# Kernel optimization log

Measured on AMD Instinct MI355X. Metric: run time of the kernel, lower is better.

## Reference

```python
import jax, jax.numpy as jnp
import numpy as np

L, B, H = 4096, 32, 512


def setup_inputs() -> dict:
    key = jax.random.key(0)
    k1, k2, k3, k4 = jax.random.split(key, 4)
    query = jax.random.normal(k1, (B, H), dtype=jnp.float32)
    key_val = jax.random.normal(k2, (L, B, H), dtype=jnp.float32)
    # torch Linear(2H, H, bias=False): weight is (H, 2H); we store transposed (2H, H)
    W = jax.random.normal(k3, (2 * H, H), dtype=jnp.float32) * (1.0 / np.sqrt(2 * H))
    v = jax.random.normal(k4, (H,), dtype=jnp.float32)
    return {"query": query, "key_val": key_val, "W": W, "v": v}


def reference(query, key_val, W, v):
    # concat([expand(query), key], -1) @ W == query @ W_q + key @ W_k
    Wq, Wk = W[:H], W[H:]                       # each (H, H)
    q_proj = query @ Wq                          # (B, H)
    k_proj = jnp.einsum('lbi,ih->lbh', key_val, Wk)  # (L, B, H)
    energy = jnp.tanh(q_proj[None, :, :] + k_proj)   # (L, B, H)
    scores = jnp.einsum('h,lbh->bl', v, energy)      # (B, L)
    return jax.nn.softmax(scores, axis=1)[:, None, :]  # (B, 1, L)
```

## Files before the change

### kernel.cpp

```cpp
#include <hip/hip_runtime.h>
#include <hip/hip_bf16.h>
#include <stdint.h>

#define L_DIM 4096
#define B_DIM 32
#define H_DIM 512
#define M_DIM (L_DIM * B_DIM)
#define K_DIM H_DIM

typedef _Float16 half8 __attribute__((ext_vector_type(8)));
typedef __fp16 fp16x2 __attribute__((ext_vector_type(2)));
typedef float floatx4 __attribute__((ext_vector_type(4)));

__device__ __forceinline__ float tanh_fast(float x) {
  float e = __builtin_amdgcn_exp2f(x * 2.88539008177793f);
  return 1.0f - 2.0f * __builtin_amdgcn_rcpf(e + 1.0f);
}

__device__ __forceinline__ void async_copy16(const _Float16* g, _Float16* l) {
  __builtin_amdgcn_global_load_lds(
      (__attribute__((address_space(1))) unsigned int*)(const_cast<_Float16*>(g)),
      (__attribute__((address_space(3))) unsigned int*)(l),
      16, 0, 0);
}

__global__ __launch_bounds__(128) void qproj_kernel(const float* __restrict__ query,
                                                    const float* __restrict__ W,
                                                    float* __restrict__ qp) {
  const int b = blockIdx.x;
  const int h = threadIdx.x * 4;
  const float* qrow = query + b * H_DIM;
  float4 acc = make_float4(0.f, 0.f, 0.f, 0.f);
#pragma unroll 8
  for (int i = 0; i < K_DIM; ++i) {
    const float qv = qrow[i];
    const float4 w4 = *(const float4*)(W + (size_t)i * H_DIM + h);
    acc.x += qv * w4.x; acc.y += qv * w4.y;
    acc.z += qv * w4.z; acc.w += qv * w4.w;
  }
  *(float4*)(qp + (size_t)b * H_DIM + h) = acc;
}

__global__ __launch_bounds__(256) void wconv_kernel(const float* __restrict__ W,
                                                    _Float16* __restrict__ W2) {
  const int t = blockIdx.x * 256 + threadIdx.x;
  const int s = t & 3;
  const int n = (t >> 2) & 511;
  const int kt = t >> 11;
  const int kseg = s ^ ((n >> 1) & 3);
  const int kbase = H_DIM + kt * 32 + kseg * 8;
  half8 h;
#pragma unroll
  for (int j = 0; j < 8; ++j)
    h[j] = (_Float16)W[(size_t)(kbase + j) * H_DIM + n];
  *(half8*)(W2 + (size_t)t * 8) = h;
}

__global__ __launch_bounds__(256, 2) void fused_gemm_kernel(
    const float* __restrict__ key, const _Float16* __restrict__ W2,
    const float* __restrict__ qp, const float* __restrict__ v,
    float* __restrict__ scores) {
  __shared__ __align__(16) _Float16 As[64 * 40];
  __shared__ __align__(16) _Float16 Bs[512 * 32];
  __shared__ float swave[256];

  const int tid = threadIdx.x;
  const int lane = tid & 63;
  const int w = tid >> 6;
  const int l15 = lane & 15;
  const int quad = lane >> 4;
  const int m0 = blockIdx.x * 64;

  const int am = tid >> 2;
  const int aks = (tid & 3) * 8;
  const float* ag = key + (size_t)(m0 + am) * K_DIM + aks;
  _Float16* asdst = As + am * 40 + aks;

  const _Float16* bg = W2 + (size_t)(w * 64 + lane) * 8;
  _Float16* bdst0 = Bs + (size_t)(w * 64) * 8;

  int aoff[4];
#pragma unroll
  for (int fm = 0; fm < 4; ++fm) aoff[fm] = (fm * 16 + l15) * 40 + quad * 8;
  int boff[8];
#pragma unroll
  for (int fn = 0; fn < 8; ++fn) {
    const int n = w * 128 + fn * 16 + l15;
    boff[fn] = n * 32 + (quad ^ ((n >> 1) & 3)) * 8;
  }

  floatx4 acc[4][8];
#pragma unroll
  for (int fm = 0; fm < 4; ++fm)
#pragma unroll
    for (int fn = 0; fn < 8; ++fn) acc[fm][fn] = (floatx4)0.0f;

  for (int kt = 0; kt < 16; ++kt) {
    const float4 f0 = *(const float4*)(ag + kt * 32);
    const float4 f1 = *(const float4*)(ag + kt * 32 + 4);
    __syncthreads();
    const fp16x2 p0 = __builtin_amdgcn_cvt_pkrtz(f0.x, f0.y);
    const fp16x2 p1 = __builtin_amdgcn_cvt_pkrtz(f0.z, f0.w);
    const fp16x2 p2 = __builtin_amdgcn_cvt_pkrtz(f1.x, f1.y);
    const fp16x2 p3 = __builtin_amdgcn_cvt_pkrtz(f1.z, f1.w);
    uint4 u;
    u.x = __builtin_bit_cast(unsigned, p0);
    u.y = __builtin_bit_cast(unsigned, p1);
    u.z = __builtin_bit_cast(unsigned, p2);
    u.w = __builtin_bit_cast(unsigned, p3);
    *(uint4*)asdst = u;
    const _Float16* bsrc = bg + (size_t)kt * 16384;
#pragma unroll
    for (int c = 0; c < 8; ++c) async_copy16(bsrc + c * 2048, bdst0 + c * 2048);
    __syncthreads();

    half8 av[4];
#pragma unroll
    for (int fm = 0; fm < 4; ++fm) av[fm] = *(const half8*)(As + aoff[fm]);
    half8 bv[8];
#pragma unroll
    for (int fn = 0; fn < 8; ++fn) bv[fn] = *(const half8*)(Bs + boff[fn]);
#pragma unroll
    for (int fm = 0; fm < 4; ++fm)
#pragma unroll
      for (int fn = 0; fn < 8; ++fn)
        acc[fm][fn] = __builtin_amdgcn_mfma_f32_16x16x32_f16(av[fm], bv[fn],
                                                             acc[fm][fn], 0, 0, 0);
  }

  float vv[8];
#pragma unroll
  for (int fn = 0; fn < 8; ++fn) vv[fn] = v[w * 128 + fn * 16 + l15];

#pragma unroll
  for (int fm = 0; fm < 4; ++fm) {
#pragma unroll
    for (int r = 0; r < 4; ++r) {
      const int mrow = fm * 16 + quad * 4 + r;
      const float* qrow = qp + (size_t)(mrow & 31) * H_DIM;
      float rs = 0.f;
#pragma unroll
      for (int fn = 0; fn < 8; ++fn) {
        const int n = w * 128 + fn * 16 + l15;
        const float x = qrow[n] + acc[fm][fn][r];
        rs += vv[fn] * tanh_fast(x);
      }
      rs += __shfl_xor(rs, 1);
      rs += __shfl_xor(rs, 2);
      rs += __shfl_xor(rs, 4);
      rs += __shfl_xor(rs, 8);
      if (l15 == 0) swave[w * 64 + mrow] = rs;
    }
  }
  __syncthreads();
  if (tid < 64) {
    const float s = swave[tid] + swave[64 + tid] + swave[128 + tid] + swave[192 + tid];
    scores[(size_t)m0 + tid] = s;
  }
}

__global__ __launch_bounds__(256) void softmax_kernel(const float* __restrict__ scores,
                                                      float* __restrict__ out) {
  const int b = blockIdx.x;
  const int t = threadIdx.x;
  __shared__ float red[256];
  float s[16];
#pragma unroll
  for (int i = 0; i < 16; ++i) s[i] = scores[(size_t)(t + i * 256) * B_DIM + b];
  float mx = s[0];
#pragma unroll
  for (int i = 1; i < 16; ++i) mx = fmaxf(mx, s[i]);
  red[t] = mx;
  __syncthreads();
  for (int off = 128; off > 0; off >>= 1) {
    if (t < off) red[t] = fmaxf(red[t], red[t + off]);
    __syncthreads();
  }
  mx = red[0];
  __syncthreads();
  float sum = 0.f;
#pragma unroll
  for (int i = 0; i < 16; ++i) {
    s[i] = __builtin_amdgcn_exp2f((s[i] - mx) * 1.44269504f);
    sum += s[i];
  }
  red[t] = sum;
  __syncthreads();
  for (int off = 128; off > 0; off >>= 1) {
    if (t < off) red[t] += red[t + off];
    __syncthreads();
  }
  const float inv = 1.0f / red[0];
#pragma unroll
  for (int i = 0; i < 16; ++i) out[(size_t)b * L_DIM + t + i * 256] = s[i] * inv;
}

extern "C" void kernel_launch(void* const* d_in, const int* in_sizes, int n_in,
                              void* d_out, int out_size, void* d_ws, size_t ws_size,
                              hipStream_t stream) {
  const float* query = (const float*)d_in[0];
  const float* key   = (const float*)d_in[1];
  const float* W     = (const float*)d_in[2];
  const float* v     = (const float*)d_in[3];
  float* out = (float*)d_out;

  char* ws = (char*)d_ws;
  float* qp       = (float*)ws;
  float* scores   = (float*)(ws + 65536);
  _Float16* W2    = (_Float16*)(ws + 65536 + 524288);

  qproj_kernel<<<32, 128, 0, stream>>>(query, W, qp);
  wconv_kernel<<<128, 256, 0, stream>>>(W, W2);
  fused_gemm_kernel<<<M_DIM / 64, 256, 0, stream>>>(key, W2, qp, v, scores);
  softmax_kernel<<<B_DIM, 256, 0, stream>>>(scores, out);
}
```

Before: 456.5 us.

## Load GEMM operands directly into registers, dropping LDS staging and barriers

The fused GEMM kernel no longer stages A and B tiles through shared memory. Each lane now loads its key rows straight from global memory, converts them to fp16 in registers and prefetches the next k-tile. W2 is re-laid out in MFMA fragment order so B fragments come from coalesced global loads. Scores are stored transposed so the softmax reads contiguously. This removes the per-tile barriers and LDS traffic, but every wave now fetches the full B panel from global memory or L2 instead of sharing it through LDS, and the A loads are strided.

Result: slower. 540.1 us (+18.3%).

```diff
diff --git a/kernel.cpp b/kernel.cpp
--- a/kernel.cpp
+++ b/kernel.cpp
@@ -17,11 +17,13 @@
   return 1.0f - 2.0f * __builtin_amdgcn_rcpf(e + 1.0f);
 }
 
-__device__ __forceinline__ void async_copy16(const _Float16* g, _Float16* l) {
-  __builtin_amdgcn_global_load_lds(
-      (__attribute__((address_space(1))) unsigned int*)(const_cast<_Float16*>(g)),
-      (__attribute__((address_space(3))) unsigned int*)(l),
-      16, 0, 0);
+__device__ __forceinline__ half8 pack8(const float4& f0, const float4& f1) {
+  const fp16x2 p0 = __builtin_amdgcn_cvt_pkrtz(f0.x, f0.y);
+  const fp16x2 p1 = __builtin_amdgcn_cvt_pkrtz(f0.z, f0.w);
+  const fp16x2 p2 = __builtin_amdgcn_cvt_pkrtz(f1.x, f1.y);
+  const fp16x2 p3 = __builtin_amdgcn_cvt_pkrtz(f1.z, f1.w);
+  struct { fp16x2 a, b, c, d; } s{p0, p1, p2, p3};
+  return __builtin_bit_cast(half8, s);
 }
 
 __global__ __launch_bounds__(128) void qproj_kernel(const float* __restrict__ query,
@@ -44,11 +46,12 @@
 __global__ __launch_bounds__(256) void wconv_kernel(const float* __restrict__ W,
                                                     _Float16* __restrict__ W2) {
   const int t = blockIdx.x * 256 + threadIdx.x;
-  const int s = t & 3;
-  const int n = (t >> 2) & 511;
+  const int l15 = t & 15;
+  const int q = (t >> 4) & 3;
+  const int nc = (t >> 6) & 31;
   const int kt = t >> 11;
-  const int kseg = s ^ ((n >> 1) & 3);
-  const int kbase = H_DIM + kt * 32 + kseg * 8;
+  const int n = nc * 16 + l15;
+  const int kbase = H_DIM + kt * 32 + q * 8;
   half8 h;
 #pragma unroll
   for (int j = 0; j < 8; ++j)
@@ -60,8 +63,6 @@
     const float* __restrict__ key, const _Float16* __restrict__ W2,
     const float* __restrict__ qp, const float* __restrict__ v,
     float* __restrict__ scores) {
-  __shared__ __align__(16) _Float16 As[64 * 40];
-  __shared__ __align__(16) _Float16 Bs[512 * 32];
   __shared__ float swave[256];
 
   const int tid = threadIdx.x;
@@ -71,23 +72,12 @@
   const int quad = lane >> 4;
   const int m0 = blockIdx.x * 64;
 
-  const int am = tid >> 2;
-  const int aks = (tid & 3) * 8;
-  const float* ag = key + (size_t)(m0 + am) * K_DIM + aks;
-  _Float16* asdst = As + am * 40 + aks;
-
-  const _Float16* bg = W2 + (size_t)(w * 64 + lane) * 8;
-  _Float16* bdst0 = Bs + (size_t)(w * 64) * 8;
-
-  int aoff[4];
-#pragma unroll
-  for (int fm = 0; fm < 4; ++fm) aoff[fm] = (fm * 16 + l15) * 40 + quad * 8;
-  int boff[8];
-#pragma unroll
-  for (int fn = 0; fn < 8; ++fn) {
-    const int n = w * 128 + fn * 16 + l15;
-    boff[fn] = n * 32 + (quad ^ ((n >> 1) & 3)) * 8;
-  }
+  const float* aptr[4];
+#pragma unroll
+  for (int fm = 0; fm < 4; ++fm)
+    aptr[fm] = key + (size_t)(m0 + fm * 16 + l15) * K_DIM + quad * 8;
+
+  const half8* bptr = (const half8*)W2 + (size_t)(w * 8) * 64 + lane;
 
   floatx4 acc[4][8];
 #pragma unroll
@@ -95,31 +85,43 @@
 #pragma unroll
     for (int fn = 0; fn < 8; ++fn) acc[fm][fn] = (floatx4)0.0f;
 
-  for (int kt = 0; kt < 16; ++kt) {
-    const float4 f0 = *(const float4*)(ag + kt * 32);
-    const float4 f1 = *(const float4*)(ag + kt * 32 + 4);
-    __syncthreads();
-    const fp16x2 p0 = __builtin_amdgcn_cvt_pkrtz(f0.x, f0.y);
-    const fp16x2 p1 = __builtin_amdgcn_cvt_pkrtz(f0.z, f0.w);
-    const fp16x2 p2 = __builtin_amdgcn_cvt_pkrtz(f1.x, f1.y);
-    const fp16x2 p3 = __builtin_amdgcn_cvt_pkrtz(f1.z, f1.w);
-    uint4 u;
-    u.x = __builtin_bit_cast(unsigned, p0);
-    u.y = __builtin_bit_cast(unsigned, p1);
-    u.z = __builtin_bit_cast(unsigned, p2);
-    u.w = __builtin_bit_cast(unsigned, p3);
-    *(uint4*)asdst = u;
-    const _Float16* bsrc = bg + (size_t)kt * 16384;
-#pragma unroll
-    for (int c = 0; c < 8; ++c) async_copy16(bsrc + c * 2048, bdst0 + c * 2048);
-    __syncthreads();
-
+  float4 ra0[4], ra1[4];
+#pragma unroll
+  for (int fm = 0; fm < 4; ++fm) {
+    ra0[fm] = *(const float4*)(aptr[fm]);
+    ra1[fm] = *(const float4*)(aptr[fm] + 4);
+    aptr[fm] += 32;
+  }
+
+#pragma unroll 3
+  for (int kt = 0; kt < 15; ++kt) {
+    half8 bv[8];
+#pragma unroll
+    for (int fn = 0; fn < 8; ++fn) bv[fn] = bptr[fn * 64];
+    bptr += 32 * 64;
     half8 av[4];
 #pragma unroll
-    for (int fm = 0; fm < 4; ++fm) av[fm] = *(const half8*)(As + aoff[fm]);
+    for (int fm = 0; fm < 4; ++fm) av[fm] = pack8(ra0[fm], ra1[fm]);
+#pragma unroll
+    for (int fm = 0; fm < 4; ++fm) {
+      ra0[fm] = *(const float4*)(aptr[fm]);
+      ra1[fm] = *(const float4*)(aptr[fm] + 4);
+      aptr[fm] += 32;
+    }
+#pragma unroll
+    for (int fm = 0; fm < 4; ++fm)
+#pragma unroll
+      for (int fn = 0; fn < 8; ++fn)
+        acc[fm][fn] = __builtin_amdgcn_mfma_f32_16x16x32_f16(av[fm], bv[fn],
+                                                             acc[fm][fn], 0, 0, 0);
+  }
+  {
     half8 bv[8];
 #pragma unroll
-    for (int fn = 0; fn < 8; ++fn) bv[fn] = *(const half8*)(Bs + boff[fn]);
+    for (int fn = 0; fn < 8; ++fn) bv[fn] = bptr[fn * 64];
+    half8 av[4];
+#pragma unroll
+    for (int fm = 0; fm < 4; ++fm) av[fm] = pack8(ra0[fm], ra1[fm]);
 #pragma unroll
     for (int fm = 0; fm < 4; ++fm)
 #pragma unroll
@@ -155,7 +157,8 @@
   __syncthreads();
   if (tid < 64) {
     const float s = swave[tid] + swave[64 + tid] + swave[128 + tid] + swave[192 + tid];
-    scores[(size_t)m0 + tid] = s;
+    const int m = m0 + tid;
+    scores[(size_t)(m & 31) * L_DIM + (m >> 5)] = s;
   }
 }
 
@@ -164,9 +167,10 @@
   const int b = blockIdx.x;
   const int t = threadIdx.x;
   __shared__ float red[256];
+  const float* srow = scores + (size_t)b * L_DIM;
   float s[16];
 #pragma unroll
-  for (int i = 0; i < 16; ++i) s[i] = scores[(size_t)(t + i * 256) * B_DIM + b];
+  for (int i = 0; i < 16; ++i) s[i] = srow[t + i * 256];
   float mx = s[0];
 #pragma unroll
   for (int i = 1; i < 16; ++i) mx = fmaxf(mx, s[i]);
```
